# Optimization experiments

Hardware: AMD Instinct MI355X
Metric: run time of the kernel (lower is better)

## Reference

```python
import jax, jax.numpy as jnp
import numpy as np

EPS = 1e-8
V_LAMBDA = 1.0
T_LAMBDA = 1.0
BB, DIM = 8192, 256


def _rowwise_cos(a, b):
    # torch.cosine_similarity semantics: dot / (max(|a|,eps) * max(|b|,eps))
    na = jnp.maximum(jnp.linalg.norm(a, axis=-1), EPS)
    nb = jnp.maximum(jnp.linalg.norm(b, axis=-1), EPS)
    return jnp.sum(a * b, axis=-1) / (na * nb)


def _clamped_normalize(x):
    n = jnp.maximum(jnp.linalg.norm(x, axis=-1, keepdims=True), EPS)
    return x / n


def _retrieval_acc(sim, labels):
    # sim: [v, t]; top-1 retrieval accuracy in percent
    return jnp.mean((jnp.argmax(sim, axis=-1) == labels).astype(jnp.float32)) * 100.0


def setup_inputs() -> dict:
    key = jax.random.key(0)
    ks = jax.random.split(key, 5)
    names = ['vis_pred', 'text_pred', 'vis_feats_proj', 'caption_emb', 'vis_feats_proj_narr']
    return {n: jax.random.normal(k, (BB, DIM), dtype=jnp.float32) for n, k in zip(names, ks)}


def reference(vis_pred, text_pred, vis_feats_proj, caption_emb, vis_feats_proj_narr):
    bb = vis_pred.shape[0]
    labels = jnp.arange(bb)

    # training losses (row-wise cosine similarity)
    vis_loss = jnp.mean(1.0 - _rowwise_cos(vis_pred, vis_feats_proj))
    text_loss = jnp.mean(1.0 - _rowwise_cos(text_pred, caption_emb))
    loss = V_LAMBDA * vis_loss + T_LAMBDA * text_loss

    # retrieval accuracies (no_grad block). The torch repeat_interleave/repeat +
    # elementwise cosine construction is exactly the pairwise cosine-sim matrix:
    # normalize rows once, then a [bb, dim] x [dim, bb] GEMM.
    v = _clamped_normalize(jax.lax.stop_gradient(vis_pred))
    gt_v = _clamped_normalize(jax.lax.stop_gradient(vis_feats_proj))
    narr_v = _clamped_normalize(jax.lax.stop_gradient(vis_feats_proj_narr))
    gt_t = _clamped_normalize(jax.lax.stop_gradient(caption_emb))
    # NOTE: in the original code both t_r and gt_t_r are tiles of gt_text, so
    # the 'text' side of every sim matrix is gt_t. We reproduce that faithfully.

    acc_gtv_gtt = _retrieval_acc(jnp.einsum('vd,td->vt', gt_v, gt_t), labels)
    acc_v_gtt = _retrieval_acc(jnp.einsum('vd,td->vt', v, gt_t), labels)
    acc_gtv_t = _retrieval_acc(jnp.einsum('vd,td->vt', gt_v, gt_t), labels)
    acc_v_t = _retrieval_acc(jnp.einsum('vd,td->vt', v, gt_t), labels)
    acc_narr_gtt = _retrieval_acc(jnp.einsum('vd,td->vt', narr_v, gt_t), labels)
    acc_narr_t = _retrieval_acc(jnp.einsum('vd,td->vt', narr_v, gt_t), labels)

    # order: vis_loss, text_loss, loss, gt_v-gt_t, v-gt_t, gt_v-t, v-t, narr_v-gt_t, narr_v-t
    return jnp.stack([vis_loss, text_loss, loss,
                      acc_gtv_gtt, acc_v_gtt, acc_gtv_t, acc_v_t,
                      acc_narr_gtt, acc_narr_t])
```

## Files before the change

### kernel.cpp

```cpp
#include <hip/hip_runtime.h>
#include <hip/hip_bf16.h>
#include <stdint.h>
#include <limits.h>

#define BB 8192
#define DIM 256

typedef __attribute__((ext_vector_type(4))) int int32x4;

__device__ __forceinline__ void load_lds16(const char* g, char* l) {
  __builtin_amdgcn_global_load_lds(
      (const __attribute__((address_space(1))) unsigned int*)g,
      (__attribute__((address_space(3))) unsigned int*)l, 16, 0, 0);
}

__device__ __forceinline__ float q8f(float x) {
  return rintf(fmaxf(fminf(x * 256.f, 127.f), -127.f));
}

__device__ __forceinline__ int imax(int a, int b) { return a > b ? a : b; }

__device__ __forceinline__ int dpp_max16(int u) {
  int t;
  t = __builtin_amdgcn_update_dpp(0, u, 0xB1, 0xF, 0xF, true);
  u = t > u ? t : u;
  t = __builtin_amdgcn_update_dpp(0, u, 0x4E, 0xF, 0xF, true);
  u = t > u ? t : u;
  t = __builtin_amdgcn_update_dpp(0, u, 0x124, 0xF, 0xF, true);
  u = t > u ? t : u;
  t = __builtin_amdgcn_update_dpp(0, u, 0x128, 0xF, 0xF, true);
  u = t > u ? t : u;
  return u;
}

__global__ __launch_bounds__(256) void phase1(
    const float* __restrict__ vp,  const float* __restrict__ tp,
    const float* __restrict__ vfp, const float* __restrict__ ce,
    const float* __restrict__ nr,
    float* __restrict__ rowcos, int* __restrict__ diag,
    char* __restrict__ abuf,
    char* __restrict__ gtbuf,
    int* __restrict__ maxComb, float* __restrict__ sums,
    int* __restrict__ ticket) {
  __shared__ unsigned ldsT[3][4][64];
  const int wave = threadIdx.x >> 6;
  const int lane = threadIdx.x & 63;
  const int row  = blockIdx.x * 4 + wave;
  const int base = row * DIM + lane * 4;

  float4 a = *(const float4*)&vp[base];
  float4 t = *(const float4*)&tp[base];
  float4 g = *(const float4*)&vfp[base];
  float4 c = *(const float4*)&ce[base];
  float4 n = *(const float4*)&nr[base];

  float s[7];
  s[0] = a.x*a.x + a.y*a.y + a.z*a.z + a.w*a.w;
  s[1] = g.x*g.x + g.y*g.y + g.z*g.z + g.w*g.w;
  s[2] = a.x*g.x + a.y*g.y + a.z*g.z + a.w*g.w;
  s[3] = t.x*t.x + t.y*t.y + t.z*t.z + t.w*t.w;
  s[4] = c.x*c.x + c.y*c.y + c.z*c.z + c.w*c.w;
  s[5] = t.x*c.x + t.y*c.y + t.z*c.z + t.w*c.w;
  s[6] = n.x*n.x + n.y*n.y + n.z*n.z + n.w*n.w;

  #pragma unroll
  for (int mk = 1; mk < 64; mk <<= 1) {
    #pragma unroll
    for (int q = 0; q < 7; ++q) s[q] += __shfl_xor(s[q], mk);
  }

  const float eps = 1e-8f;
  float na = fmaxf(sqrtf(s[0]), eps);
  float ng = fmaxf(sqrtf(s[1]), eps);
  float nt = fmaxf(sqrtf(s[3]), eps);
  float nc = fmaxf(sqrtf(s[4]), eps);
  float nn = fmaxf(sqrtf(s[6]), eps);
  float ia = 1.f / na, ig = 1.f / ng, ic = 1.f / nc, in_ = 1.f / nn;

  float qa0=q8f(a.x*ia), qa1=q8f(a.y*ia), qa2=q8f(a.z*ia), qa3=q8f(a.w*ia);
  float qg0=q8f(g.x*ig), qg1=q8f(g.y*ig), qg2=q8f(g.z*ig), qg3=q8f(g.w*ig);
  float qn0=q8f(n.x*in_),qn1=q8f(n.y*in_),qn2=q8f(n.z*in_),qn3=q8f(n.w*in_);
  float qc0=q8f(c.x*ic), qc1=q8f(c.y*ic), qc2=q8f(c.z*ic), qc3=q8f(c.w*ic);

  float d[3];
  d[0] = qg0*qc0 + qg1*qc1 + qg2*qc2 + qg3*qc3;
  d[1] = qa0*qc0 + qa1*qc1 + qa2*qc2 + qa3*qc3;
  d[2] = qn0*qc0 + qn1*qc1 + qn2*qc2 + qn3*qc3;
  #pragma unroll
  for (int mk = 1; mk < 64; mk <<= 1) {
    #pragma unroll
    for (int q = 0; q < 3; ++q) d[q] += __shfl_xor(d[q], mk);
  }

  auto pack = [](float x0, float x1, float x2, float x3) -> unsigned {
    return ((unsigned)((int)x0 & 0xFF)) | ((unsigned)((int)x1 & 0xFF) << 8) |
           ((unsigned)((int)x2 & 0xFF) << 16) | ((unsigned)((int)x3 & 0xFF) << 24);
  };
  ((unsigned*)gtbuf)[row * 64 + lane] = pack(qc0, qc1, qc2, qc3);
  ldsT[0][wave][lane] = pack(qg0, qg1, qg2, qg3);
  ldsT[1][wave][lane] = pack(qa0, qa1, qa2, qa3);
  ldsT[2][wave][lane] = pack(qn0, qn1, qn2, qn3);

  if (lane == 0) {
    rowcos[row]        = s[2] / (na * ng);
    rowcos[BB + row]   = s[5] / (nt * nc);
    diag[0 * BB + row] = (int)d[0];
    diag[1 * BB + row] = (int)d[1];
    diag[2 * BB + row] = (int)d[2];
    maxComb[0 * BB + row] = INT_MIN;
    maxComb[1 * BB + row] = INT_MIN;
    maxComb[2 * BB + row] = INT_MIN;
  }
  if (blockIdx.x == 0 && threadIdx.x < 5) sums[threadIdx.x] = 0.f;
  if (blockIdx.x == 0 && threadIdx.x == 5) *ticket = 0;

  __syncthreads();
  if (threadIdx.x < 192) {
    int mat = threadIdx.x >> 6, l = threadIdx.x & 63;
    int kc = l >> 2, j = l & 3;
    uint4 val = *(const uint4*)&ldsT[mat][j][kc * 4];
    int tileR = blockIdx.x >> 2;
    int rm    = (blockIdx.x & 3) * 4 + j;
    *(uint4*)&abuf[(size_t)mat * BB * DIM + tileR * 4096 + kc * 256 + rm * 16] = val;
  }
}

__global__ __launch_bounds__(512, 4) void sim_argmax(
    const char* __restrict__ Af, const char* __restrict__ B,
    int* __restrict__ maxComb) {
  __shared__ char Bs[128 * 256];
  __shared__ int comb[256];

  const int tid  = threadIdx.x;
  const int lane = tid & 63;
  const int wave = tid >> 6;
  const int m    = lane & 15, quad = lane >> 4;
  const int z    = blockIdx.z;

  const int rowTile = blockIdx.y * 256;
  const int colTile = blockIdx.x * 128;
  const char* Az = Af + (size_t)z * BB * DIM +
                   ((size_t)(rowTile >> 4) + wave * 2) * 4096;
  const char* Bp = B + (size_t)colTile * DIM;

  #pragma unroll
  for (int t = 0; t < 4; ++t) {
    const int c   = t * 512 + tid;
    const int row = c >> 4;
    const int l   = (c & 15) ^ (row & 15);
    load_lds16(&Bp[row * DIM + l * 16], &Bs[c * 16]);
  }

  int32x4 af[2][2];
  #pragma unroll
  for (int rt = 0; rt < 2; ++rt)
    af[0][rt] = *(const int32x4*)&Az[(size_t)rt * 4096 + lane * 16];

  __syncthreads();

  const int rowBase  = rowTile + wave * 32;
  const int32x4 zero = (int32x4){0, 0, 0, 0};

  int32x4 acc[2][8];

  #pragma unroll
  for (int kp = 0; kp < 4; ++kp) {
    const int pb = kp & 1;
    if (kp < 3) {
      #pragma unroll
      for (int rt = 0; rt < 2; ++rt)
        af[pb ^ 1][rt] = *(const int32x4*)&Az[(size_t)rt * 4096 +
                                              (kp + 1) * 1024 + lane * 16];
    }
    int32x4 bf[8];
    #pragma unroll
    for (int ct = 0; ct < 8; ++ct) {
      int br = ct * 16 + m;
      int p  = (kp * 4 + quad) ^ m;
      bf[ct] = *(const int32x4*)&Bs[br * 256 + p * 16];
    }
    __builtin_amdgcn_s_setprio(1);
    #pragma unroll
    for (int rt = 0; rt < 2; ++rt)
      #pragma unroll
      for (int ct = 0; ct < 8; ++ct)
        acc[rt][ct] = __builtin_amdgcn_mfma_i32_16x16x64_i8(
            af[pb][rt], bf[ct], (kp == 0) ? zero : acc[rt][ct], 0, 0, 0);
    __builtin_amdgcn_s_setprio(0);
  }

  if ((blockIdx.x >> 1) != blockIdx.y) {
    const int addOne = ((int)blockIdx.y > (int)(blockIdx.x >> 1)) ? 1 : 0;
    #pragma unroll
    for (int rt = 0; rt < 2; ++rt) {
      #pragma unroll
      for (int reg = 0; reg < 4; ++reg) {
        int u = imax(imax(imax(acc[rt][0][reg], acc[rt][1][reg]),
                          imax(acc[rt][2][reg], acc[rt][3][reg])),
                     imax(imax(acc[rt][4][reg], acc[rt][5][reg]),
                          imax(acc[rt][6][reg], acc[rt][7][reg])));
        u = dpp_max16(u);
        if (m == 0)
          comb[wave * 32 + rt * 16 + quad * 4 + reg] = u * 2 + addOne;
      }
    }
  } else {
    #pragma unroll
    for (int rt = 0; rt < 2; ++rt) {
      #pragma unroll
      for (int reg = 0; reg < 4; ++reg) {
        const int i = rowBase + rt * 16 + quad * 4 + reg;
        int u = INT_MIN;
        #pragma unroll
        for (int ct = 0; ct < 8; ++ct) {
          const int j = colTile + ct * 16 + m;
          int w = acc[rt][ct][reg] * 2 + ((j < i) ? 1 : 0);
          w = (j == i) ? INT_MIN : w;
          u = imax(u, w);
        }
        u = dpp_max16(u);
        if (m == 0) comb[wave * 32 + rt * 16 + quad * 4 + reg] = u;
      }
    }
  }

  __syncthreads();
  if (tid < 256)
    atomicMax(&maxComb[(size_t)z * BB + rowTile + tid], comb[tid]);
}

__global__ __launch_bounds__(256) void phase3_fin(
    const int* __restrict__ diag, const int* __restrict__ maxComb,
    const float* __restrict__ rowcos,
    float* __restrict__ sums, int* __restrict__ ticket,
    float* __restrict__ out) {
  __shared__ float red[4][5];
  __shared__ bool amLast;
  int r = blockIdx.x * 256 + threadIdx.x;
  int lane = threadIdx.x & 63, wave = threadIdx.x >> 6;
  float v[5];
  v[0] = rowcos[r];
  v[1] = rowcos[BB + r];
  #pragma unroll
  for (int z = 0; z < 3; ++z)
    v[2 + z] = (2 * diag[z * BB + r] >= maxComb[z * BB + r]) ? 1.f : 0.f;
  #pragma unroll
  for (int mk = 1; mk < 64; mk <<= 1) {
    #pragma unroll
    for (int q = 0; q < 5; ++q) v[q] += __shfl_xor(v[q], mk);
  }
  if (lane == 0) {
    #pragma unroll
    for (int q = 0; q < 5; ++q) red[wave][q] = v[q];
  }
  __syncthreads();
  if (threadIdx.x < 5) {
    float acc = red[0][threadIdx.x] + red[1][threadIdx.x] +
                red[2][threadIdx.x] + red[3][threadIdx.x];
    atomicAdd(&sums[threadIdx.x], acc);
  }
  __threadfence();
  __syncthreads();
  if (threadIdx.x == 0)
    amLast = (atomicAdd(ticket, 1) == (int)gridDim.x - 1);
  __syncthreads();
  if (amLast && threadIdx.x == 0) {
    float s0 = atomicAdd(&sums[0], 0.f);
    float s1 = atomicAdd(&sums[1], 0.f);
    float s2 = atomicAdd(&sums[2], 0.f);
    float s3 = atomicAdd(&sums[3], 0.f);
    float s4 = atomicAdd(&sums[4], 0.f);
    float vl = 1.f - s0 * (1.f / BB);
    float tl = 1.f - s1 * (1.f / BB);
    out[0] = vl;
    out[1] = tl;
    out[2] = vl + tl;
    float a0 = s2 * (100.f / BB);
    float a1 = s3 * (100.f / BB);
    float a2 = s4 * (100.f / BB);
    out[3] = a0;
    out[4] = a1;
    out[5] = a0;
    out[6] = a1;
    out[7] = a2;
    out[8] = a2;
  }
}

extern "C" void kernel_launch(void* const* d_in, const int* in_sizes, int n_in,
                              void* d_out, int out_size, void* d_ws, size_t ws_size,
                              hipStream_t stream) {
  const float* vp  = (const float*)d_in[0];
  const float* tp  = (const float*)d_in[1];
  const float* vfp = (const float*)d_in[2];
  const float* ce  = (const float*)d_in[3];
  const float* nr  = (const float*)d_in[4];

  char* ws = (char*)d_ws;
  float* sums    = (float*)ws;
  int*   ticket  = (int*)(ws + 32);
  int*   maxComb = (int*)(ws + 64);
  int*   diag    = maxComb + 3 * BB;
  float* rowcos  = (float*)(diag + 3 * BB);
  char*  abuf    = (char*)(rowcos + 2 * BB);
  char*  gtbuf   = abuf + (size_t)3 * BB * DIM;


  phase1<<<BB / 4, 256, 0, stream>>>(vp, tp, vfp, ce, nr, rowcos, diag,
                                     abuf, gtbuf, maxComb, sums, ticket);

  dim3 grid(64, 32, 3);
  sim_argmax<<<grid, 512, 0, stream>>>(abuf, gtbuf, maxComb);

  phase3_fin<<<BB / 256, 256, 0, stream>>>(diag, maxComb, rowcos, sums, ticket,
                                           (float*)d_out);
}
```

Baseline: 142.1 us.

## Process four column tiles per block with double-buffered B loads

Each sim_argmax block now walks four 128-column tiles instead of one, prefetching the next B tile into a second LDS buffer while computing the current one. Per-tile row maxima are kept in LDS and merged before a single atomicMax per row, so the grid shrinks fourfold. This aims to hide B load latency, amortize A-fragment loads and cut global atomics. In exchange LDS per block doubles to about 68KB, which may reduce occupancy, and the per-tile loop adds a barrier on each iteration.

```diff
diff --git a/kernel.cpp b/kernel.cpp
--- a/kernel.cpp
+++ b/kernel.cpp
@@ -128,8 +128,8 @@
 __global__ __launch_bounds__(512, 4) void sim_argmax(
     const char* __restrict__ Af, const char* __restrict__ B,
     int* __restrict__ maxComb) {
-  __shared__ char Bs[128 * 256];
-  __shared__ int comb[256];
+  __shared__ char Bs[2][128 * 256];
+  __shared__ int comb[4][256];
 
   const int tid  = threadIdx.x;
   const int lane = tid & 63;
@@ -138,95 +138,118 @@
   const int z    = blockIdx.z;
 
   const int rowTile = blockIdx.y * 256;
-  const int colTile = blockIdx.x * 128;
+  const int xt0     = blockIdx.x * 4;
+
   const char* Az = Af + (size_t)z * BB * DIM +
                    ((size_t)(rowTile >> 4) + wave * 2) * 4096;
-  const char* Bp = B + (size_t)colTile * DIM;
-
-  #pragma unroll
-  for (int t = 0; t < 4; ++t) {
-    const int c   = t * 512 + tid;
-    const int row = c >> 4;
-    const int l   = (c & 15) ^ (row & 15);
-    load_lds16(&Bp[row * DIM + l * 16], &Bs[c * 16]);
-  }
-
+
+  {
+    const char* Bp = B + (size_t)xt0 * 128 * DIM;
+    #pragma unroll
+    for (int t = 0; t < 4; ++t) {
+      const int c   = t * 512 + tid;
+      const int row = c >> 4;
+      const int l   = (c & 15) ^ (row & 15);
+      load_lds16(&Bp[row * DIM + l * 16], &Bs[0][c * 16]);
+    }
+  }
   int32x4 af[2][2];
   #pragma unroll
   for (int rt = 0; rt < 2; ++rt)
     af[0][rt] = *(const int32x4*)&Az[(size_t)rt * 4096 + lane * 16];
-
   __syncthreads();
 
   const int rowBase  = rowTile + wave * 32;
   const int32x4 zero = (int32x4){0, 0, 0, 0};
 
-  int32x4 acc[2][8];
-
-  #pragma unroll
-  for (int kp = 0; kp < 4; ++kp) {
-    const int pb = kp & 1;
-    if (kp < 3) {
+  #pragma unroll 1
+  for (int xl = 0; xl < 4; ++xl) {
+    const int cur = xl & 1;
+    const int xt  = xt0 + xl;
+
+    if (xl < 3) {
+      const char* Bp = B + ((size_t)xt + 1) * 128 * DIM;
+      #pragma unroll
+      for (int t = 0; t < 4; ++t) {
+        const int c   = t * 512 + tid;
+        const int row = c >> 4;
+        const int l   = (c & 15) ^ (row & 15);
+        load_lds16(&Bp[row * DIM + l * 16], &Bs[cur ^ 1][c * 16]);
+      }
+    }
+
+    int32x4 acc[2][8];
+    #pragma unroll
+    for (int kp = 0; kp < 4; ++kp) {
+      const int pb = kp & 1;
+      {
+        const int kn = (kp + 1) & 3;
+        #pragma unroll
+        for (int rt = 0; rt < 2; ++rt)
+          af[pb ^ 1][rt] = *(const int32x4*)&Az[(size_t)rt * 4096 +
+                                                kn * 1024 + lane * 16];
+      }
+      int32x4 bf[8];
+      #pragma unroll
+      for (int ct = 0; ct < 8; ++ct) {
+        int br = ct * 16 + m;
+        int p  = (kp * 4 + quad) ^ m;
+        bf[ct] = *(const int32x4*)&Bs[cur][br * 256 + p * 16];
+      }
+      __builtin_amdgcn_s_setprio(1);
       #pragma unroll
       for (int rt = 0; rt < 2; ++rt)
-        af[pb ^ 1][rt] = *(const int32x4*)&Az[(size_t)rt * 4096 +
-                                              (kp + 1) * 1024 + lane * 16];
+        #pragma unroll
+        for (int ct = 0; ct < 8; ++ct)
+          acc[rt][ct] = __builtin_amdgcn_mfma_i32_16x16x64_i8(
+              af[pb][rt], bf[ct], (kp == 0) ? zero : acc[rt][ct], 0, 0, 0);
+      __builtin_amdgcn_s_setprio(0);
     }
-    int32x4 bf[8];
-    #pragma unroll
-    for (int ct = 0; ct < 8; ++ct) {
-      int br = ct * 16 + m;
-      int p  = (kp * 4 + quad) ^ m;
-      bf[ct] = *(const int32x4*)&Bs[br * 256 + p * 16];
+
+    const int colTile = xt * 128;
+    if ((xt >> 1) != (int)blockIdx.y) {
+      const int addOne = ((int)blockIdx.y > (xt >> 1)) ? 1 : 0;
+      #pragma unroll
+      for (int rt = 0; rt < 2; ++rt) {
+        #pragma unroll
+        for (int reg = 0; reg < 4; ++reg) {
+          int u = imax(imax(imax(acc[rt][0][reg], acc[rt][1][reg]),
+                            imax(acc[rt][2][reg], acc[rt][3][reg])),
+                       imax(imax(acc[rt][4][reg], acc[rt][5][reg]),
+                            imax(acc[rt][6][reg], acc[rt][7][reg])));
+          u = dpp_max16(u);
+          if (m == 0)
+            comb[xl][wave * 32 + rt * 16 + quad * 4 + reg] = u * 2 + addOne;
+        }
+      }
+    } else {
+      #pragma unroll
+      for (int rt = 0; rt < 2; ++rt) {
+        #pragma unroll
+        for (int reg = 0; reg < 4; ++reg) {
+          const int i = rowBase + rt * 16 + quad * 4 + reg;
+          int u = INT_MIN;
+          #pragma unroll
+          for (int ct = 0; ct < 8; ++ct) {
+            const int j = colTile + ct * 16 + m;
+            int w = acc[rt][ct][reg] * 2 + ((j < i) ? 1 : 0);
+            w = (j == i) ? INT_MIN : w;
+            u = imax(u, w);
+          }
+          u = dpp_max16(u);
+          if (m == 0) comb[xl][wave * 32 + rt * 16 + quad * 4 + reg] = u;
+        }
+      }
     }
-    __builtin_amdgcn_s_setprio(1);
-    #pragma unroll
-    for (int rt = 0; rt < 2; ++rt)
-      #pragma unroll
-      for (int ct = 0; ct < 8; ++ct)
-        acc[rt][ct] = __builtin_amdgcn_mfma_i32_16x16x64_i8(
-            af[pb][rt], bf[ct], (kp == 0) ? zero : acc[rt][ct], 0, 0, 0);
-    __builtin_amdgcn_s_setprio(0);
-  }
-
-  if ((blockIdx.x >> 1) != blockIdx.y) {
-    const int addOne = ((int)blockIdx.y > (int)(blockIdx.x >> 1)) ? 1 : 0;
-    #pragma unroll
-    for (int rt = 0; rt < 2; ++rt) {
-      #pragma unroll
-      for (int reg = 0; reg < 4; ++reg) {
-        int u = imax(imax(imax(acc[rt][0][reg], acc[rt][1][reg]),
-                          imax(acc[rt][2][reg], acc[rt][3][reg])),
-                     imax(imax(acc[rt][4][reg], acc[rt][5][reg]),
-                          imax(acc[rt][6][reg], acc[rt][7][reg])));
-        u = dpp_max16(u);
-        if (m == 0)
-          comb[wave * 32 + rt * 16 + quad * 4 + reg] = u * 2 + addOne;
-      }
-    }
-  } else {
-    #pragma unroll
-    for (int rt = 0; rt < 2; ++rt) {
-      #pragma unroll
-      for (int reg = 0; reg < 4; ++reg) {
-        const int i = rowBase + rt * 16 + quad * 4 + reg;
-        int u = INT_MIN;
-        #pragma unroll
-        for (int ct = 0; ct < 8; ++ct) {
-          const int j = colTile + ct * 16 + m;
-          int w = acc[rt][ct][reg] * 2 + ((j < i) ? 1 : 0);
-          w = (j == i) ? INT_MIN : w;
-          u = imax(u, w);
-        }
-        u = dpp_max16(u);
-        if (m == 0) comb[wave * 32 + rt * 16 + quad * 4 + reg] = u;
-      }
-    }
-  }
-
-  __syncthreads();
-  if (tid < 256)
-    atomicMax(&maxComb[(size_t)z * BB + rowTile + tid], comb[tid]);
+
+    __syncthreads();
+  }
+
+  if (tid < 256) {
+    int u = imax(imax(comb[0][tid], comb[1][tid]),
+                 imax(comb[2][tid], comb[3][tid]));
+    atomicMax(&maxComb[(size_t)z * BB + rowTile + tid], u);
+  }
 }
 
 __global__ __launch_bounds__(256) void phase3_fin(
@@ -309,7 +332,7 @@
   phase1<<<BB / 4, 256, 0, stream>>>(vp, tp, vfp, ce, nr, rowcos, diag,
                                      abuf, gtbuf, maxComb, sums, ticket);
 
-  dim3 grid(64, 32, 3);
+  dim3 grid(16, 32, 3);
   sim_argmax<<<grid, 512, 0, stream>>>(abuf, gtbuf, maxComb);
 
   phase3_fin<<<BB / 256, 256, 0, stream>>>(diag, maxComb, rowcos, sums, ticket,
```

Result: slower. 249.6 us (+75.6%).
